# Kernel optimization log

Measured on AMD Instinct MI355X. Metric: run time of the kernel, lower is better.

The kernel has to match this reference:

```python
import jax, jax.numpy as jnp
import numpy as np

HEADS = 12
DIM_HEAD = 64

def setup_inputs() -> dict:
    key = jax.random.key(0)
    ks = jax.random.split(key, 5)
    B, S, D = 4, 2048, 768
    s = 0.02
    return {
        "x": jax.random.normal(ks[0], (B, S, D), dtype=jnp.float32),
        "Wq": jax.random.normal(ks[1], (D, D), dtype=jnp.float32) * s,
        "Wk": jax.random.normal(ks[2], (D, D), dtype=jnp.float32) * s,
        "Wv": jax.random.normal(ks[3], (D, D), dtype=jnp.float32) * s,
        "Wo": jax.random.normal(ks[4], (D, D), dtype=jnp.float32) * s,
        "bo": jnp.zeros((D,), dtype=jnp.float32),
    }

def reference(x, Wq, Wk, Wv, Wo, bo):
    B, S, D = x.shape
    H, Dh = HEADS, DIM_HEAD
    scale = Dh ** -0.5
    # projections (torch Linear: x @ W^T)
    q = (x @ Wq.T).reshape(B, S, H, Dh).transpose(0, 2, 1, 3) * scale  # [B,H,S,Dh]
    k = (x @ Wk.T).reshape(B, S, H, Dh).transpose(0, 2, 1, 3)
    v = (x @ Wv.T).reshape(B, S, H, Dh).transpose(0, 2, 1, 3)
    sim = jnp.einsum("bhid,bhjd->bhij", q, k)  # [B,H,S,S]
    mask_value = -jnp.finfo(sim.dtype).max
    causal_mask = jnp.triu(jnp.ones((S, S), dtype=bool), k=1)
    sim = jnp.where(causal_mask, mask_value, sim)
    attn = jax.nn.softmax(sim, axis=-1)
    # dropout is identity in eval mode
    out = jnp.einsum("bhij,bhjd->bhid", attn, v)  # [B,H,S,Dh]
    out = out.transpose(0, 2, 1, 3).reshape(B, S, H * Dh)
    return out @ Wo.T + bo
```

## Files before the change

kernel.cpp:

```cpp
#include <hip/hip_runtime.h>
#include <stdint.h>

typedef unsigned short u16;
typedef __bf16 bf16x8 __attribute__((ext_vector_type(8)));
typedef float f32x4 __attribute__((ext_vector_type(4)));
typedef u16 u16x4 __attribute__((ext_vector_type(4)));
typedef u16 u16x8 __attribute__((ext_vector_type(8)));
typedef uint32_t u32x2 __attribute__((ext_vector_type(2)));

#define LDS_CAST(p) (reinterpret_cast<__attribute__((address_space(3))) uint32_t*>(reinterpret_cast<uintptr_t>(p)))
#define GLB_CAST(p) (reinterpret_cast<const __attribute__((address_space(1))) uint32_t*>(reinterpret_cast<uintptr_t>(p)))
#define GLOAD16(g, l) __builtin_amdgcn_global_load_lds(GLB_CAST(g), LDS_CAST(l), 16, 0, 0)
#define AS3U16(p) (reinterpret_cast<__attribute__((address_space(3))) u16*>(reinterpret_cast<uintptr_t>(p)))

__device__ __forceinline__ u16 f2bf(float f) {
    uint32_t u = __builtin_bit_cast(uint32_t, f);
    u += 0x7fffu + ((u >> 16) & 1u);
    return (u16)(u >> 16);
}
__device__ __forceinline__ u16 bfbits(float f) {
    return __builtin_bit_cast(u16, (__bf16)f);
}

__global__ void cast_f32_bf16(const float* __restrict__ in, u16* __restrict__ out, int n4) {
    int i = blockIdx.x * blockDim.x + threadIdx.x;
    if (i >= n4) return;
    float4 f = reinterpret_cast<const float4*>(in)[i];
    u16x4 o;
    o.x = f2bf(f.x); o.y = f2bf(f.y); o.z = f2bf(f.z); o.w = f2bf(f.w);
    reinterpret_cast<u16x4*>(out)[i] = o;
}

__global__ void cast_w4(const float* __restrict__ a, const float* __restrict__ b,
                        const float* __restrict__ c, const float* __restrict__ d,
                        u16* __restrict__ oa, u16* __restrict__ ob,
                        u16* __restrict__ oc, u16* __restrict__ od, int n4) {
    const int z = blockIdx.y;
    const float* in = (z == 0) ? a : (z == 1) ? b : (z == 2) ? c : d;
    u16* out = (z == 0) ? oa : (z == 1) ? ob : (z == 2) ? oc : od;
    int i = blockIdx.x * blockDim.x + threadIdx.x;
    if (i >= n4) return;
    float4 f = reinterpret_cast<const float4*>(in)[i];
    u16x4 o;
    o.x = f2bf(f.x); o.y = f2bf(f.y); o.z = f2bf(f.z); o.w = f2bf(f.w);
    reinterpret_cast<u16x4*>(out)[i] = o;
}

__global__ __launch_bounds__(256) void gemm_qkv(
    const u16* __restrict__ X, const u16* __restrict__ Wq,
    const u16* __restrict__ Wk, const u16* __restrict__ Wv,
    u16* __restrict__ qo, u16* __restrict__ ko, u16* __restrict__ vTo)
{
    __shared__ u16 As[2][128 * 32];
    __shared__ u16 Bs[2][128 * 32];
    const int tid = threadIdx.x;
    const int lane = tid & 63;
    const int w = tid >> 6;
    const int lr = lane & 15, lg = lane >> 4;
    const int wrow = (w >> 1) * 64, wcol = (w & 1) * 64;
    const int row0 = blockIdx.y * 128, col0 = blockIdx.x * 128;
    const int z = blockIdx.z;
    const u16* Wt = (z == 0) ? Wq : (z == 1) ? Wk : Wv;

    f32x4 acc[4][4];
#pragma unroll
    for (int m = 0; m < 4; ++m)
#pragma unroll
        for (int n = 0; n < 4; ++n)
#pragma unroll
            for (int j = 0; j < 4; ++j) acc[m][n][j] = 0.f;

#define QSTAGE(KT, BUF)                                                                            \
    {                                                                                              \
        _Pragma("unroll")                                                                          \
        for (int it = 0; it < 2; ++it) {                                                           \
            const int c = it * 256 + w * 64 + lane;                                                \
            const int row = c >> 2, c16 = c & 3;                                                   \
            GLOAD16(X  + (size_t)(row0 + row) * 768 + (KT) * 32 + c16 * 8, &As[BUF][(it * 256 + w * 64) * 8]); \
            GLOAD16(Wt + (size_t)(col0 + row) * 768 + (KT) * 32 + c16 * 8, &Bs[BUF][(it * 256 + w * 64) * 8]); \
        }                                                                                          \
    }

    QSTAGE(0, 0);
    for (int kt = 0; kt < 24; ++kt) {
        const int cur = kt & 1;
        __syncthreads();
        if (kt < 23) QSTAGE(kt + 1, cur ^ 1);
        bf16x8 af[4], bfr[4];
#pragma unroll
        for (int m = 0; m < 4; ++m) af[m] = *(const bf16x8*)&As[cur][(wrow + m * 16 + lr) * 32 + lg * 8];
#pragma unroll
        for (int n = 0; n < 4; ++n) bfr[n] = *(const bf16x8*)&Bs[cur][(wcol + n * 16 + lr) * 32 + lg * 8];
#pragma unroll
        for (int m = 0; m < 4; ++m)
#pragma unroll
            for (int n = 0; n < 4; ++n)
                acc[m][n] = __builtin_amdgcn_mfma_f32_16x16x32_bf16(af[m], bfr[n], acc[m][n], 0, 0, 0);
    }
#undef QSTAGE

    if (z == 2) {
#pragma unroll
        for (int n = 0; n < 4; ++n) {
            const int j = col0 + wcol + n * 16 + lr;
            const int h = j >> 6, dh = j & 63;
#pragma unroll
            for (int m = 0; m < 4; ++m) {
                const int i0 = row0 + wrow + m * 16 + lg * 4;
                const int b = i0 >> 11, s0 = i0 & 2047;
                u16x4 pk;
#pragma unroll
                for (int r = 0; r < 4; ++r) pk[r] = bfbits(acc[m][n][r]);
                *(u16x4*)&vTo[(((size_t)b * 12 + h) * 64 + dh) * 2048 + s0] = pk;
            }
        }
    } else {
        u16* outp = (z == 0) ? qo : ko;
        const float scl = (z == 0) ? 0.18033688011112042f : 1.0f;
#pragma unroll
        for (int n = 0; n < 4; ++n) {
            const int j = col0 + wcol + n * 16 + lr;
            const int h = j >> 6, dh = j & 63;
#pragma unroll
            for (int m = 0; m < 4; ++m)
#pragma unroll
                for (int r = 0; r < 4; ++r) {
                    const int i = row0 + wrow + m * 16 + lg * 4 + r;
                    const int b = i >> 11, s = i & 2047;
                    outp[(((size_t)b * 12 + h) * 2048 + s) * 64 + dh] = bfbits(acc[m][n][r] * scl);
                }
        }
    }
}

template<bool DIAG>
__device__ __forceinline__ void attn_step(
    const bf16x8* aq, f32x4* o, float* lrow,
    const u16* __restrict__ Ksb, const u16* __restrict__ Vsb, u16* __restrict__ PT,
    int kvb, int qg0, int lr, int lg)
{
    f32x4 sacc[4];
#pragma unroll
    for (int n = 0; n < 4; ++n)
#pragma unroll
        for (int j = 0; j < 4; ++j) sacc[n][j] = 0.f;
    __builtin_amdgcn_s_setprio(1);
#pragma unroll
    for (int kk = 0; kk < 2; ++kk)
#pragma unroll
        for (int n = 0; n < 4; ++n) {
            const int row = n * 16 + lr;
            const int p = (kk * 4 + lg) ^ (row & 7);
            bf16x8 bk = *(const bf16x8*)&Ksb[row * 64 + p * 8];
            sacc[n] = __builtin_amdgcn_mfma_f32_16x16x32_bf16(aq[kk], bk, sacc[n], 0, 0, 0);
        }
    __builtin_amdgcn_s_setprio(0);

    float pv[4][4];
#pragma unroll
    for (int r = 0; r < 4; ++r) {
        float ls = 0.f;
#pragma unroll
        for (int n = 0; n < 4; ++n) {
            float sv = sacc[n][r];
            if (DIAG && (kvb + n * 16 + lr) > qg0 + r) sv = -1e30f;
            const float e = __builtin_amdgcn_exp2f(sv);
            pv[r][n] = e;
            ls += e;
        }
        lrow[r] += ls;
    }

#pragma unroll
    for (int n = 0; n < 4; ++n) {
        u16x4 pk;
#pragma unroll
        for (int r = 0; r < 4; ++r) pk[r] = bfbits(pv[r][n]);
        *(u16x4*)&PT[(n * 16 + lr) * 16 + lg * 4] = pk;
    }

    u32x2 t0, t1, t2, t3;
    __attribute__((address_space(3))) u16* pb = AS3U16(PT) + lg * 128 + lr * 4;
    asm volatile("ds_read_b64_tr_b16 %0, %1" : "=v"(t0) : "v"(pb) : "memory");
    asm volatile("ds_read_b64_tr_b16 %0, %1 offset:128" : "=v"(t1) : "v"(pb) : "memory");
    asm volatile("ds_read_b64_tr_b16 %0, %1 offset:1024" : "=v"(t2) : "v"(pb) : "memory");
    asm volatile("ds_read_b64_tr_b16 %0, %1 offset:1152" : "=v"(t3) : "v"(pb) : "memory");
    asm volatile("s_waitcnt lgkmcnt(0)" ::: "memory");
    __builtin_amdgcn_sched_barrier(0);
    union { u32x2 h[2]; bf16x8 v; } ua, ub;
    ua.h[0] = t0; ua.h[1] = t1;
    ub.h[0] = t2; ub.h[1] = t3;
    const bf16x8 ap0 = ua.v, ap1 = ub.v;

    __builtin_amdgcn_s_setprio(1);
#pragma unroll
    for (int n = 0; n < 4; ++n) {
        const int rowv = n * 16 + lr;
        const int p0 = (0 + lg) ^ (rowv & 7);
        const int p1 = (4 + lg) ^ (rowv & 7);
        bf16x8 bv0 = *(const bf16x8*)&Vsb[rowv * 64 + p0 * 8];
        bf16x8 bv1 = *(const bf16x8*)&Vsb[rowv * 64 + p1 * 8];
        o[n] = __builtin_amdgcn_mfma_f32_16x16x32_bf16(ap0, bv0, o[n], 0, 0, 0);
        o[n] = __builtin_amdgcn_mfma_f32_16x16x32_bf16(ap1, bv1, o[n], 0, 0, 0);
    }
    __builtin_amdgcn_s_setprio(0);
}

__global__ __launch_bounds__(256) void attn_kernel(
    const u16* __restrict__ q, const u16* __restrict__ k,
    const u16* __restrict__ vT, u16* __restrict__ attn)
{
    __shared__ u16 Ks[2][64 * 64];
    __shared__ u16 Vs[2][64 * 64];
    __shared__ u16 Ps[4][64 * 16];

    const int pair = blockIdx.x, bh = blockIdx.y;
    const int qA = pair, qB = 31 - pair;
    const int tid = threadIdx.x, lane = tid & 63, w = tid >> 6;
    const int lr = lane & 15, lg = lane >> 4;

    const u16* Kp = k + (size_t)bh * 2048 * 64;
    const u16* Vp = vT + (size_t)bh * 64 * 2048;

    const u16* QpA = q + ((size_t)bh * 2048 + qA * 64 + w * 16) * 64;
    const u16* QpB = q + ((size_t)bh * 2048 + qB * 64 + w * 16) * 64;
    bf16x8 aqA[2], aqB[2];
    aqA[0] = *(const bf16x8*)&QpA[lr * 64 + lg * 8];
    aqA[1] = *(const bf16x8*)&QpA[lr * 64 + 32 + lg * 8];
    aqB[0] = *(const bf16x8*)&QpB[lr * 64 + lg * 8];
    aqB[1] = *(const bf16x8*)&QpB[lr * 64 + 32 + lg * 8];

    f32x4 oA[4], oB[4];
    float lA[4], lB[4];
#pragma unroll
    for (int n = 0; n < 4; ++n)
#pragma unroll
        for (int j = 0; j < 4; ++j) { oA[n][j] = 0.f; oB[n][j] = 0.f; }
#pragma unroll
    for (int r = 0; r < 4; ++r) { lA[r] = 0.f; lB[r] = 0.f; }

#define STAGE(T, BUF)                                                                        \
    {                                                                                        \
        _Pragma("unroll")                                                                    \
        for (int it = 0; it < 2; ++it) {                                                     \
            const int c = it * 256 + w * 64 + lane;                                          \
            const int row = c >> 3, pc = c & 7;                                              \
            const int lc = pc ^ (row & 7);                                                   \
            GLOAD16(Kp + (size_t)((T) * 64 + row) * 64 + lc * 8, &Ks[BUF][(it * 256 + w * 64) * 8]); \
            GLOAD16(Vp + (size_t)row * 2048 + (T) * 64 + lc * 8, &Vs[BUF][(it * 256 + w * 64) * 8]); \
        }                                                                                    \
    }

    STAGE(0, 0);
    const int qg0A = qA * 64 + w * 16 + lg * 4;
    const int qg0B = qB * 64 + w * 16 + lg * 4;

    int t = 0;
    for (; t < qA; ++t) {
        const int cur = t & 1;
        __syncthreads();
        STAGE(t + 1, cur ^ 1);
        attn_step<false>(aqB, oB, lB, Ks[cur], Vs[cur], Ps[w], t * 64, qg0B, lr, lg);
        attn_step<false>(aqA, oA, lA, Ks[cur], Vs[cur], Ps[w], t * 64, qg0A, lr, lg);
    }
    {
        const int cur = t & 1;
        __syncthreads();
        STAGE(t + 1, cur ^ 1);
        attn_step<false>(aqB, oB, lB, Ks[cur], Vs[cur], Ps[w], t * 64, qg0B, lr, lg);
        attn_step<true >(aqA, oA, lA, Ks[cur], Vs[cur], Ps[w], t * 64, qg0A, lr, lg);
        ++t;
    }
    for (; t < qB; ++t) {
        const int cur = t & 1;
        __syncthreads();
        STAGE(t + 1, cur ^ 1);
        attn_step<false>(aqB, oB, lB, Ks[cur], Vs[cur], Ps[w], t * 64, qg0B, lr, lg);
    }
    {
        const int cur = t & 1;
        __syncthreads();
        attn_step<true >(aqB, oB, lB, Ks[cur], Vs[cur], Ps[w], t * 64, qg0B, lr, lg);
    }
#undef STAGE

#pragma unroll
    for (int r = 0; r < 4; ++r) {
#pragma unroll
        for (int off = 1; off < 16; off <<= 1) {
            lA[r] += __shfl_xor(lA[r], off);
            lB[r] += __shfl_xor(lB[r], off);
        }
        lA[r] = 1.f / lA[r];
        lB[r] = 1.f / lB[r];
    }

    const int b = bh / 12, h = bh - b * 12;
#pragma unroll
    for (int n = 0; n < 4; ++n)
#pragma unroll
        for (int r = 0; r < 4; ++r) {
            const int sA = qA * 64 + w * 16 + lg * 4 + r;
            const int sB = qB * 64 + w * 16 + lg * 4 + r;
            attn[((size_t)b * 2048 + sA) * 768 + h * 64 + n * 16 + lr] = bfbits(oA[n][r] * lA[r]);
            attn[((size_t)b * 2048 + sB) * 768 + h * 64 + n * 16 + lr] = bfbits(oB[n][r] * lB[r]);
        }
}

__global__ __launch_bounds__(256) void gemm_out(
    const u16* __restrict__ A, const u16* __restrict__ Wo,
    const float* __restrict__ bo, float* __restrict__ out)
{
    __shared__ u16 As[2][128 * 32];
    __shared__ u16 Bs[2][128 * 32];
    const int tid = threadIdx.x;
    const int lane = tid & 63;
    const int w = tid >> 6;
    const int lr = lane & 15, lg = lane >> 4;
    const int wrow = (w >> 1) * 64, wcol = (w & 1) * 64;
    const int row0 = blockIdx.y * 128, col0 = blockIdx.x * 128;

    f32x4 acc[4][4];
#pragma unroll
    for (int m = 0; m < 4; ++m)
#pragma unroll
        for (int n = 0; n < 4; ++n)
#pragma unroll
            for (int j = 0; j < 4; ++j) acc[m][n][j] = 0.f;

#define OSTAGE(KT, BUF)                                                                            \
    {                                                                                              \
        _Pragma("unroll")                                                                          \
        for (int it = 0; it < 2; ++it) {                                                           \
            const int c = it * 256 + w * 64 + lane;                                                \
            const int row = c >> 2, c16 = c & 3;                                                   \
            GLOAD16(A  + (size_t)(row0 + row) * 768 + (KT) * 32 + c16 * 8, &As[BUF][(it * 256 + w * 64) * 8]); \
            GLOAD16(Wo + (size_t)(col0 + row) * 768 + (KT) * 32 + c16 * 8, &Bs[BUF][(it * 256 + w * 64) * 8]); \
        }                                                                                          \
    }

    OSTAGE(0, 0);
    for (int kt = 0; kt < 24; ++kt) {
        const int cur = kt & 1;
        __syncthreads();
        if (kt < 23) OSTAGE(kt + 1, cur ^ 1);
        bf16x8 af[4], bfr[4];
#pragma unroll
        for (int m = 0; m < 4; ++m) af[m] = *(const bf16x8*)&As[cur][(wrow + m * 16 + lr) * 32 + lg * 8];
#pragma unroll
        for (int n = 0; n < 4; ++n) bfr[n] = *(const bf16x8*)&Bs[cur][(wcol + n * 16 + lr) * 32 + lg * 8];
#pragma unroll
        for (int m = 0; m < 4; ++m)
#pragma unroll
            for (int n = 0; n < 4; ++n)
                acc[m][n] = __builtin_amdgcn_mfma_f32_16x16x32_bf16(af[m], bfr[n], acc[m][n], 0, 0, 0);
    }
#undef OSTAGE

#pragma unroll
    for (int n = 0; n < 4; ++n) {
        const int j = col0 + wcol + n * 16 + lr;
        const float bj = bo[j];
#pragma unroll
        for (int m = 0; m < 4; ++m)
#pragma unroll
            for (int r = 0; r < 4; ++r) {
                const int i = row0 + wrow + m * 16 + lg * 4 + r;
                out[(size_t)i * 768 + j] = acc[m][n][r] + bj;
            }
    }
}

extern "C" void kernel_launch(void* const* d_in, const int* in_sizes, int n_in,
                              void* d_out, int out_size, void* d_ws, size_t ws_size,
                              hipStream_t stream) {
    const float* x  = (const float*)d_in[0];
    const float* Wq = (const float*)d_in[1];
    const float* Wk = (const float*)d_in[2];
    const float* Wv = (const float*)d_in[3];
    const float* Wo = (const float*)d_in[4];
    const float* bo = (const float*)d_in[5];
    float* out = (float*)d_out;

    const size_t NX = 6291456;
    const size_t NW = 589824;
    if (ws_size < (NX * 4 + NW * 4 + NX) * sizeof(u16)) return;
    u16* ws  = (u16*)d_ws;
    u16* xb  = ws;
    u16* wqb = xb  + NX;
    u16* wkb = wqb + NW;
    u16* wvb = wkb + NW;
    u16* wob = wvb + NW;
    u16* qb_ = wob + NW;
    u16* kb_ = qb_ + NX;
    u16* vtb = kb_ + NX;
    u16* ab_ = vtb + NX;

    cast_f32_bf16<<<6144, 256, 0, stream>>>(x, xb, (int)(NX / 4));
    cast_w4<<<dim3(576, 4), 256, 0, stream>>>(Wq, Wk, Wv, Wo, wqb, wkb, wvb, wob, (int)(NW / 4));

    gemm_qkv<<<dim3(6, 64, 3), 256, 0, stream>>>(xb, wqb, wkb, wvb, qb_, kb_, vtb);
    attn_kernel<<<dim3(16, 48), 256, 0, stream>>>(qb_, kb_, vtb, ab_);
    gemm_out<<<dim3(6, 64), 256, 0, stream>>>(ab_, wob, bo, out);
}
```

Measured before the change: 138.9 us.

## Triple-buffer GEMM loads with explicit vmcnt waits; fuse dual-tile attention steps

The QKV and output-projection GEMMs move from a double-buffered to a three-stage LDS ring. Each step waits with an explicit vmcnt count and uses raw barriers, so two future K-tiles stay in flight while the current tile is computed. The attention inner step now processes both query tiles (A and B) in one call, so K and V fragments read from LDS are shared by the two MFMA chains instead of being read twice. The cost is more LDS per GEMM block and more live registers in the attention kernel, which can lower occupancy.

```diff
diff --git a/kernel.cpp b/kernel.cpp
--- a/kernel.cpp
+++ b/kernel.cpp
@@ -51,8 +51,8 @@
     const u16* __restrict__ Wk, const u16* __restrict__ Wv,
     u16* __restrict__ qo, u16* __restrict__ ko, u16* __restrict__ vTo)
 {
-    __shared__ u16 As[2][128 * 32];
-    __shared__ u16 Bs[2][128 * 32];
+    __shared__ u16 As[3][128 * 32];
+    __shared__ u16 Bs[3][128 * 32];
     const int tid = threadIdx.x;
     const int lane = tid & 63;
     const int w = tid >> 6;
@@ -70,33 +70,45 @@
 #pragma unroll
             for (int j = 0; j < 4; ++j) acc[m][n][j] = 0.f;
 
-#define QSTAGE(KT, BUF)                                                                            \
+#define QSTAGE(KT)                                                                                 \
     {                                                                                              \
+        const int buf_ = (KT) % 3;                                                                 \
         _Pragma("unroll")                                                                          \
         for (int it = 0; it < 2; ++it) {                                                           \
             const int c = it * 256 + w * 64 + lane;                                                \
             const int row = c >> 2, c16 = c & 3;                                                   \
-            GLOAD16(X  + (size_t)(row0 + row) * 768 + (KT) * 32 + c16 * 8, &As[BUF][(it * 256 + w * 64) * 8]); \
-            GLOAD16(Wt + (size_t)(col0 + row) * 768 + (KT) * 32 + c16 * 8, &Bs[BUF][(it * 256 + w * 64) * 8]); \
+            GLOAD16(X  + (size_t)(row0 + row) * 768 + (KT) * 32 + c16 * 8, &As[buf_][(it * 256 + w * 64) * 8]); \
+            GLOAD16(Wt + (size_t)(col0 + row) * 768 + (KT) * 32 + c16 * 8, &Bs[buf_][(it * 256 + w * 64) * 8]); \
         }                                                                                          \
     }
 
-    QSTAGE(0, 0);
-    for (int kt = 0; kt < 24; ++kt) {
-        const int cur = kt & 1;
-        __syncthreads();
-        if (kt < 23) QSTAGE(kt + 1, cur ^ 1);
-        bf16x8 af[4], bfr[4];
-#pragma unroll
-        for (int m = 0; m < 4; ++m) af[m] = *(const bf16x8*)&As[cur][(wrow + m * 16 + lr) * 32 + lg * 8];
-#pragma unroll
-        for (int n = 0; n < 4; ++n) bfr[n] = *(const bf16x8*)&Bs[cur][(wcol + n * 16 + lr) * 32 + lg * 8];
-#pragma unroll
-        for (int m = 0; m < 4; ++m)
-#pragma unroll
-            for (int n = 0; n < 4; ++n)
-                acc[m][n] = __builtin_amdgcn_mfma_f32_16x16x32_bf16(af[m], bfr[n], acc[m][n], 0, 0, 0);
-    }
+#define QSTEP(KT, VN, PF)                                                                          \
+    {                                                                                              \
+        asm volatile("s_waitcnt vmcnt(" #VN ")" ::: "memory");                                     \
+        __builtin_amdgcn_s_barrier();                                                              \
+        const int cur_ = (KT) % 3;                                                                 \
+        bf16x8 af[4], bfr[4];                                                                      \
+        _Pragma("unroll")                                                                          \
+        for (int m = 0; m < 4; ++m) af[m] = *(const bf16x8*)&As[cur_][(wrow + m * 16 + lr) * 32 + lg * 8]; \
+        _Pragma("unroll")                                                                          \
+        for (int n = 0; n < 4; ++n) bfr[n] = *(const bf16x8*)&Bs[cur_][(wcol + n * 16 + lr) * 32 + lg * 8]; \
+        asm volatile("s_waitcnt lgkmcnt(0)" ::: "memory");                                         \
+        __builtin_amdgcn_sched_barrier(0);                                                         \
+        __builtin_amdgcn_s_barrier();                                                              \
+        if (PF) QSTAGE((KT) + 3);                                                                  \
+        _Pragma("unroll")                                                                          \
+        for (int m = 0; m < 4; ++m)                                                                \
+            _Pragma("unroll")                                                                      \
+            for (int n = 0; n < 4; ++n)                                                            \
+                acc[m][n] = __builtin_amdgcn_mfma_f32_16x16x32_bf16(af[m], bfr[n], acc[m][n], 0, 0, 0); \
+    }
+
+    QSTAGE(0); QSTAGE(1); QSTAGE(2);
+    for (int kt = 0; kt < 21; ++kt) QSTEP(kt, 8, true);
+    QSTEP(21, 8, false);
+    QSTEP(22, 4, false);
+    QSTEP(23, 0, false);
+#undef QSTEP
 #undef QSTAGE
 
     if (z == 2) {
@@ -133,17 +145,19 @@
     }
 }
 
-template<bool DIAG>
-__device__ __forceinline__ void attn_step(
-    const bf16x8* aq, f32x4* o, float* lrow,
+template<bool DO_A, bool DIAG>
+__device__ __forceinline__ void attn_step2(
+    const bf16x8* aqA, const bf16x8* aqB,
+    f32x4* oA, f32x4* oB, float* lA, float* lB,
     const u16* __restrict__ Ksb, const u16* __restrict__ Vsb, u16* __restrict__ PT,
-    int kvb, int qg0, int lr, int lg)
+    int kvb, int qg0A, int qg0B, int lr, int lg)
 {
-    f32x4 sacc[4];
+    f32x4 sA[4], sB[4];
 #pragma unroll
     for (int n = 0; n < 4; ++n)
 #pragma unroll
-        for (int j = 0; j < 4; ++j) sacc[n][j] = 0.f;
+        for (int j = 0; j < 4; ++j) { sB[n][j] = 0.f; if (DO_A) sA[n][j] = 0.f; }
+
     __builtin_amdgcn_s_setprio(1);
 #pragma unroll
     for (int kk = 0; kk < 2; ++kk)
@@ -152,45 +166,79 @@
             const int row = n * 16 + lr;
             const int p = (kk * 4 + lg) ^ (row & 7);
             bf16x8 bk = *(const bf16x8*)&Ksb[row * 64 + p * 8];
-            sacc[n] = __builtin_amdgcn_mfma_f32_16x16x32_bf16(aq[kk], bk, sacc[n], 0, 0, 0);
+            sB[n] = __builtin_amdgcn_mfma_f32_16x16x32_bf16(aqB[kk], bk, sB[n], 0, 0, 0);
+            if (DO_A) sA[n] = __builtin_amdgcn_mfma_f32_16x16x32_bf16(aqA[kk], bk, sA[n], 0, 0, 0);
         }
     __builtin_amdgcn_s_setprio(0);
 
-    float pv[4][4];
+    float pvB[4][4], pvA[4][4];
 #pragma unroll
     for (int r = 0; r < 4; ++r) {
         float ls = 0.f;
 #pragma unroll
         for (int n = 0; n < 4; ++n) {
-            float sv = sacc[n][r];
-            if (DIAG && (kvb + n * 16 + lr) > qg0 + r) sv = -1e30f;
+            float sv = sB[n][r];
+            if (!DO_A && DIAG && (kvb + n * 16 + lr) > qg0B + r) sv = -1e30f;
             const float e = __builtin_amdgcn_exp2f(sv);
-            pv[r][n] = e;
+            pvB[r][n] = e;
             ls += e;
         }
-        lrow[r] += ls;
-    }
-
+        lB[r] += ls;
+    }
+    if (DO_A) {
+#pragma unroll
+        for (int r = 0; r < 4; ++r) {
+            float ls = 0.f;
+#pragma unroll
+            for (int n = 0; n < 4; ++n) {
+                float sv = sA[n][r];
+                if (DIAG && (kvb + n * 16 + lr) > qg0A + r) sv = -1e30f;
+                const float e = __builtin_amdgcn_exp2f(sv);
+                pvA[r][n] = e;
+                ls += e;
+            }
+            lA[r] += ls;
+        }
+    }
+
+    __attribute__((address_space(3))) u16* pb = AS3U16(PT) + lg * 128 + lr * 4;
+    u32x2 b0, b1, b2, b3, a0, a1, a2, a3;
 #pragma unroll
     for (int n = 0; n < 4; ++n) {
         u16x4 pk;
 #pragma unroll
-        for (int r = 0; r < 4; ++r) pk[r] = bfbits(pv[r][n]);
+        for (int r = 0; r < 4; ++r) pk[r] = bfbits(pvB[r][n]);
         *(u16x4*)&PT[(n * 16 + lr) * 16 + lg * 4] = pk;
     }
-
-    u32x2 t0, t1, t2, t3;
-    __attribute__((address_space(3))) u16* pb = AS3U16(PT) + lg * 128 + lr * 4;
-    asm volatile("ds_read_b64_tr_b16 %0, %1" : "=v"(t0) : "v"(pb) : "memory");
-    asm volatile("ds_read_b64_tr_b16 %0, %1 offset:128" : "=v"(t1) : "v"(pb) : "memory");
-    asm volatile("ds_read_b64_tr_b16 %0, %1 offset:1024" : "=v"(t2) : "v"(pb) : "memory");
-    asm volatile("ds_read_b64_tr_b16 %0, %1 offset:1152" : "=v"(t3) : "v"(pb) : "memory");
+    asm volatile("ds_read_b64_tr_b16 %0, %1" : "=v"(b0) : "v"(pb) : "memory");
+    asm volatile("ds_read_b64_tr_b16 %0, %1 offset:128" : "=v"(b1) : "v"(pb) : "memory");
+    asm volatile("ds_read_b64_tr_b16 %0, %1 offset:1024" : "=v"(b2) : "v"(pb) : "memory");
+    asm volatile("ds_read_b64_tr_b16 %0, %1 offset:1152" : "=v"(b3) : "v"(pb) : "memory");
+    if (DO_A) {
+#pragma unroll
+        for (int n = 0; n < 4; ++n) {
+            u16x4 pk;
+#pragma unroll
+            for (int r = 0; r < 4; ++r) pk[r] = bfbits(pvA[r][n]);
+            *(u16x4*)&PT[(n * 16 + lr) * 16 + lg * 4] = pk;
+        }
+        asm volatile("ds_read_b64_tr_b16 %0, %1" : "=v"(a0) : "v"(pb) : "memory");
+        asm volatile("ds_read_b64_tr_b16 %0, %1 offset:128" : "=v"(a1) : "v"(pb) : "memory");
+        asm volatile("ds_read_b64_tr_b16 %0, %1 offset:1024" : "=v"(a2) : "v"(pb) : "memory");
+        asm volatile("ds_read_b64_tr_b16 %0, %1 offset:1152" : "=v"(a3) : "v"(pb) : "memory");
+    }
     asm volatile("s_waitcnt lgkmcnt(0)" ::: "memory");
     __builtin_amdgcn_sched_barrier(0);
-    union { u32x2 h[2]; bf16x8 v; } ua, ub;
-    ua.h[0] = t0; ua.h[1] = t1;
-    ub.h[0] = t2; ub.h[1] = t3;
-    const bf16x8 ap0 = ua.v, ap1 = ub.v;
+    union { u32x2 h[2]; bf16x8 v; } u0, u1, u2, u3;
+    u0.h[0] = b0; u0.h[1] = b1;
+    u1.h[0] = b2; u1.h[1] = b3;
+    const bf16x8 apB0 = u0.v, apB1 = u1.v;
+    bf16x8 apA0, apA1;
+    if (DO_A) {
+        u2.h[0] = a0; u2.h[1] = a1;
+        u3.h[0] = a2; u3.h[1] = a3;
+        apA0 = u2.v; apA1 = u3.v;
+    }
 
     __builtin_amdgcn_s_setprio(1);
 #pragma unroll
@@ -200,8 +248,12 @@
         const int p1 = (4 + lg) ^ (rowv & 7);
         bf16x8 bv0 = *(const bf16x8*)&Vsb[rowv * 64 + p0 * 8];
         bf16x8 bv1 = *(const bf16x8*)&Vsb[rowv * 64 + p1 * 8];
-        o[n] = __builtin_amdgcn_mfma_f32_16x16x32_bf16(ap0, bv0, o[n], 0, 0, 0);
-        o[n] = __builtin_amdgcn_mfma_f32_16x16x32_bf16(ap1, bv1, o[n], 0, 0, 0);
+        oB[n] = __builtin_amdgcn_mfma_f32_16x16x32_bf16(apB0, bv0, oB[n], 0, 0, 0);
+        oB[n] = __builtin_amdgcn_mfma_f32_16x16x32_bf16(apB1, bv1, oB[n], 0, 0, 0);
+        if (DO_A) {
+            oA[n] = __builtin_amdgcn_mfma_f32_16x16x32_bf16(apA0, bv0, oA[n], 0, 0, 0);
+            oA[n] = __builtin_amdgcn_mfma_f32_16x16x32_bf16(apA1, bv1, oA[n], 0, 0, 0);
+        }
     }
     __builtin_amdgcn_s_setprio(0);
 }
@@ -260,27 +312,29 @@
         const int cur = t & 1;
         __syncthreads();
         STAGE(t + 1, cur ^ 1);
-        attn_step<false>(aqB, oB, lB, Ks[cur], Vs[cur], Ps[w], t * 64, qg0B, lr, lg);
-        attn_step<false>(aqA, oA, lA, Ks[cur], Vs[cur], Ps[w], t * 64, qg0A, lr, lg);
+        attn_step2<true, false>(aqA, aqB, oA, oB, lA, lB, Ks[cur], Vs[cur], Ps[w],
+                                t * 64, qg0A, qg0B, lr, lg);
     }
     {
         const int cur = t & 1;
         __syncthreads();
         STAGE(t + 1, cur ^ 1);
-        attn_step<false>(aqB, oB, lB, Ks[cur], Vs[cur], Ps[w], t * 64, qg0B, lr, lg);
-        attn_step<true >(aqA, oA, lA, Ks[cur], Vs[cur], Ps[w], t * 64, qg0A, lr, lg);
+        attn_step2<true, true>(aqA, aqB, oA, oB, lA, lB, Ks[cur], Vs[cur], Ps[w],
+                               t * 64, qg0A, qg0B, lr, lg);
         ++t;
     }
     for (; t < qB; ++t) {
         const int cur = t & 1;
         __syncthreads();
         STAGE(t + 1, cur ^ 1);
-        attn_step<false>(aqB, oB, lB, Ks[cur], Vs[cur], Ps[w], t * 64, qg0B, lr, lg);
+        attn_step2<false, false>(aqA, aqB, oA, oB, lA, lB, Ks[cur], Vs[cur], Ps[w],
+                                 t * 64, qg0A, qg0B, lr, lg);
     }
     {
         const int cur = t & 1;
         __syncthreads();
-        attn_step<true >(aqB, oB, lB, Ks[cur], Vs[cur], Ps[w], t * 64, qg0B, lr, lg);
+        attn_step2<false, true>(aqA, aqB, oA, oB, lA, lB, Ks[cur], Vs[cur], Ps[w],
+                                t * 64, qg0A, qg0B, lr, lg);
     }
 #undef STAGE
 
@@ -311,8 +365,8 @@
     const u16* __restrict__ A, const u16* __restrict__ Wo,
     const float* __restrict__ bo, float* __restrict__ out)
 {
-    __shared__ u16 As[2][128 * 32];
-    __shared__ u16 Bs[2][128 * 32];
+    __shared__ u16 As[3][128 * 32];
+    __shared__ u16 Bs[3][128 * 32];
     const int tid = threadIdx.x;
     const int lane = tid & 63;
     const int w = tid >> 6;
@@ -328,33 +382,45 @@
 #pragma unroll
             for (int j = 0; j < 4; ++j) acc[m][n][j] = 0.f;
 
-#define OSTAGE(KT, BUF)                                                                            \
+#define OSTAGE(KT)                                                                                 \
     {                                                                                              \
+        const int buf_ = (KT) % 3;                                                                 \
         _Pragma("unroll")                                                                          \
         for (int it = 0; it < 2; ++it) {                                                           \
             const int c = it * 256 + w * 64 + lane;                                                \
             const int row = c >> 2, c16 = c & 3;                                                   \
-            GLOAD16(A  + (size_t)(row0 + row) * 768 + (KT) * 32 + c16 * 8, &As[BUF][(it * 256 + w * 64) * 8]); \
-            GLOAD16(Wo + (size_t)(col0 + row) * 768 + (KT) * 32 + c16 * 8, &Bs[BUF][(it * 256 + w * 64) * 8]); \
+            GLOAD16(A  + (size_t)(row0 + row) * 768 + (KT) * 32 + c16 * 8, &As[buf_][(it * 256 + w * 64) * 8]); \
+            GLOAD16(Wo + (size_t)(col0 + row) * 768 + (KT) * 32 + c16 * 8, &Bs[buf_][(it * 256 + w * 64) * 8]); \
         }                                                                                          \
     }
 
-    OSTAGE(0, 0);
-    for (int kt = 0; kt < 24; ++kt) {
-        const int cur = kt & 1;
-        __syncthreads();
-        if (kt < 23) OSTAGE(kt + 1, cur ^ 1);
-        bf16x8 af[4], bfr[4];
-#pragma unroll
-        for (int m = 0; m < 4; ++m) af[m] = *(const bf16x8*)&As[cur][(wrow + m * 16 + lr) * 32 + lg * 8];
-#pragma unroll
-        for (int n = 0; n < 4; ++n) bfr[n] = *(const bf16x8*)&Bs[cur][(wcol + n * 16 + lr) * 32 + lg * 8];
-#pragma unroll
-        for (int m = 0; m < 4; ++m)
-#pragma unroll
-            for (int n = 0; n < 4; ++n)
-                acc[m][n] = __builtin_amdgcn_mfma_f32_16x16x32_bf16(af[m], bfr[n], acc[m][n], 0, 0, 0);
-    }
+#define OSTEP(KT, VN, PF)                                                                          \
+    {                                                                                              \
+        asm volatile("s_waitcnt vmcnt(" #VN ")" ::: "memory");                                     \
+        __builtin_amdgcn_s_barrier();                                                              \
+        const int cur_ = (KT) % 3;                                                                 \
+        bf16x8 af[4], bfr[4];                                                                      \
+        _Pragma("unroll")                                                                          \
+        for (int m = 0; m < 4; ++m) af[m] = *(const bf16x8*)&As[cur_][(wrow + m * 16 + lr) * 32 + lg * 8]; \
+        _Pragma("unroll")                                                                          \
+        for (int n = 0; n < 4; ++n) bfr[n] = *(const bf16x8*)&Bs[cur_][(wcol + n * 16 + lr) * 32 + lg * 8]; \
+        asm volatile("s_waitcnt lgkmcnt(0)" ::: "memory");                                         \
+        __builtin_amdgcn_sched_barrier(0);                                                         \
+        __builtin_amdgcn_s_barrier();                                                              \
+        if (PF) OSTAGE((KT) + 3);                                                                  \
+        _Pragma("unroll")                                                                          \
+        for (int m = 0; m < 4; ++m)                                                                \
+            _Pragma("unroll")                                                                      \
+            for (int n = 0; n < 4; ++n)                                                            \
+                acc[m][n] = __builtin_amdgcn_mfma_f32_16x16x32_bf16(af[m], bfr[n], acc[m][n], 0, 0, 0); \
+    }
+
+    OSTAGE(0); OSTAGE(1); OSTAGE(2);
+    for (int kt = 0; kt < 21; ++kt) OSTEP(kt, 8, true);
+    OSTEP(21, 8, false);
+    OSTEP(22, 4, false);
+    OSTEP(23, 0, false);
+#undef OSTEP
 #undef OSTAGE
 
 #pragma unroll
```

Measured after the change: 153.4 us. 1.1x slower.
